# Performance work log

Measured on AMD Instinct MI355X. Metric: run time of the kernel, lower is better.

## Reference

```python
import jax, jax.numpy as jnp
import numpy as np

B, C, D, H, W = 4, 128, 16, 16, 16
HID = 128
EPS = 1e-5


def setup_inputs() -> dict:
    key = jax.random.key(0)
    ks = jax.random.split(key, 10)
    s = 1.0 / np.sqrt(C)
    return {
        "x": jax.random.normal(ks[0], (B, C, D, H, W), dtype=jnp.float32),
        "Wq": jax.random.normal(ks[1], (HID, C), dtype=jnp.float32) * s,
        "bq": jax.random.normal(ks[2], (HID,), dtype=jnp.float32) * s,
        "Wk": jax.random.normal(ks[3], (HID, C), dtype=jnp.float32) * s,
        "bk": jax.random.normal(ks[4], (HID,), dtype=jnp.float32) * s,
        "Wv": jax.random.normal(ks[5], (HID, C), dtype=jnp.float32) * s,
        "bv": jax.random.normal(ks[6], (HID,), dtype=jnp.float32) * s,
        "bn_weight": jax.random.normal(ks[7], (HID,), dtype=jnp.float32),
        "bn_bias": jax.random.normal(ks[8], (HID,), dtype=jnp.float32),
        "gamma": jax.random.normal(ks[9], (1,), dtype=jnp.float32),
    }


def reference(x, Wq, bq, Wk, bk, Wv, bv, bn_weight, bn_bias, gamma):
    b, c, d, h, w = x.shape
    n = d * h * w
    xf = x.reshape(b, c, n)  # [B, C, N]
    # 1x1 conv3d == per-voxel linear: [B, hid, N]
    q = jnp.einsum("hc,bcn->bnh", Wq, xf) + bq  # [B, N, hid] (query permuted)
    k = jnp.einsum("hc,bcn->bhn", Wk, xf) + bk[None, :, None]  # [B, hid, N]
    v = jnp.einsum("hc,bcn->bhn", Wv, xf) + bv[None, :, None]  # [B, hid, N]
    # unscaled attention scores [B, N, N], softmax over last dim
    attn = jax.nn.softmax(jnp.einsum("bih,bhj->bij", q, k), axis=-1)
    # out[b,h,i] = sum_j v[b,h,j] * attn[b,i,j]
    out = jnp.einsum("bhj,bij->bhi", v, attn)  # [B, hid, N]
    # BatchNorm3d (training mode): per-channel stats over (B, N), biased var
    mean = jnp.mean(out, axis=(0, 2), keepdims=True)
    var = jnp.mean(jnp.square(out - mean), axis=(0, 2), keepdims=True)
    out = (out - mean) * jax.lax.rsqrt(var + EPS)
    out = out * bn_weight[None, :, None] + bn_bias[None, :, None]
    out = gamma[0] * out.reshape(b, c, d, h, w) + x
    return out
```

## Files before the change

kernel.cpp:

```cpp
#include <hip/hip_runtime.h>


#define NV 4096
#define LOG2E 1.44269504088896340736f
#define EPSV 1e-5f

typedef float f32x4 __attribute__((ext_vector_type(4)));
typedef short bf16x8 __attribute__((ext_vector_type(8)));
typedef unsigned short u16x4 __attribute__((ext_vector_type(4)));
typedef unsigned short u16x8 __attribute__((ext_vector_type(8)));
typedef unsigned int u32x2 __attribute__((ext_vector_type(2)));

static __device__ __forceinline__ unsigned short f2bf(float f) {
    union { float f; unsigned u; } v; v.f = f;
    unsigned r = v.u + 0x7FFFu + ((v.u >> 16) & 1u);
    return (unsigned short)(r >> 16);
}
static __device__ __forceinline__ float bf2f(unsigned short u) {
    union { unsigned u; float f; } v; v.u = ((unsigned)u) << 16; return v.f;
}
static __device__ __forceinline__ unsigned fbits(float f) {
    union { float f; unsigned u; } v; v.f = f; return v.u;
}

__global__ __launch_bounds__(256) void projx_kernel(
    const float* __restrict__ x,
    const float* __restrict__ Wq, const float* __restrict__ Wk,
    const float* __restrict__ Wv,
    const float* __restrict__ bq, const float* __restrict__ bk,
    const float* __restrict__ bv,
    unsigned short* __restrict__ Qb, unsigned short* __restrict__ Kb,
    unsigned short* __restrict__ Vb)
{
    __shared__ unsigned short xt[64 * 136];
    __shared__ unsigned short Wl[128 * 136];
    const int bid = blockIdx.x;
    const int m = bid >> 8, b = (bid >> 6) & 3, n0 = (bid & 63) << 6;
    const int t = threadIdx.x, w = t >> 6, lane = t & 63;
    const int quad = lane >> 4, l16 = lane & 15;

    const float* Wm = (m == 0) ? Wq : ((m == 1) ? Wk : Wv);
    const float* bias = (m == 0) ? bq : ((m == 1) ? bk : bv);

    #pragma unroll
    for (int it = 0; it < 32; ++it) {
        const int e = it * 256 + t;
        const int c = e >> 6, il = e & 63;
        xt[il * 136 + c] = f2bf(x[(((b << 7) + c) << 12) + n0 + il]);
    }
    #pragma unroll
    for (int it = 0; it < 16; ++it) {
        const int idx = it * 1024 + (t << 2);
        const float4 wv4 = *(const float4*)(Wm + idx);
        const int h = idx >> 7, c = idx & 127;
        u16x4 pk;
        pk[0] = f2bf(wv4.x); pk[1] = f2bf(wv4.y);
        pk[2] = f2bf(wv4.z); pk[3] = f2bf(wv4.w);
        *(u16x4*)(Wl + h * 136 + c) = pk;
    }
    __syncthreads();

    bf16x8 af[4];
    {
        const int il = (w << 4) + l16;
        #pragma unroll
        for (int ck = 0; ck < 4; ++ck)
            af[ck] = *(const bf16x8*)(xt + il * 136 + (ck << 5) + (quad << 3));
    }
    if (m == 2) __syncthreads();

    const int vb = n0 + (w << 4);
    unsigned short* dst = (m == 0) ? Qb : Kb;
    #pragma unroll
    for (int s = 0; s < 8; ++s) {
        const int h = (s << 4) + l16;
        f32x4 acc = {0.f, 0.f, 0.f, 0.f};
        #pragma unroll
        for (int ck = 0; ck < 4; ++ck) {
            const bf16x8 wf = *(const bf16x8*)(Wl + h * 136 + (ck << 5) + (quad << 3));
            acc = __builtin_amdgcn_mfma_f32_16x16x32_bf16(af[ck], wf, acc, 0, 0, 0);
        }
        const float bval = bias[h];
        if (m == 2) {
            #pragma unroll
            for (int r = 0; r < 4; ++r)
                xt[h * 66 + (w << 4) + (quad << 2) + r] = f2bf(acc[r] + bval);
        } else {
            #pragma unroll
            for (int r = 0; r < 4; ++r) {
                float val = acc[r] + bval;
                if (m == 0) val *= LOG2E;
                const int n = vb + (quad << 2) + r;
                dst[(((b << 12) + n) << 7) + h] = f2bf(val);
            }
        }
    }
    if (m == 2) {
        __syncthreads();
        #pragma unroll
        for (int it = 0; it < 32; ++it) {
            const int e = it * 256 + t;
            const int h = e >> 6, il = e & 63;
            Vb[(((b << 7) + h) << 12) + n0 + il] = xt[h * 66 + il];
        }
    }
}

template<int NSL>
__global__ __launch_bounds__(256, 2) void flash_kernel(
    const unsigned short* __restrict__ Qb,
    const unsigned short* __restrict__ Kb,
    const unsigned short* __restrict__ Vb,
    unsigned short* __restrict__ Opart, float* __restrict__ lpart,
    unsigned short* __restrict__ Obuf)
{
    __shared__ unsigned short Kt[64 * 128];
    __shared__ unsigned short Vt[128 * 64];
    __shared__ unsigned short pA[4][32 * 72];
    const int bid = blockIdx.x;
    const int sl = bid >> 7, b = (bid >> 5) & 3, ic = bid & 31;
    const int t = threadIdx.x, w = t >> 6, lane = t & 63;
    const int quad = lane >> 4, l16 = lane & 15;
    const int iw = (ic << 7) + (w << 5);
    const int jbase = sl * (NV / NSL);
    unsigned short* pAw = pA[w];

    const int ktg = t & 15, ktj = t >> 4;
    const int vtg = t & 7,  vth = t >> 3;
    const int kswz = (ktg ^ ktj) << 3;
    const int vswz = (vtg ^ (vth & 7)) << 3;

    bf16x8 qf[2][4];
    #pragma unroll
    for (int half = 0; half < 2; ++half) {
        const unsigned short* qp =
            Qb + (((b << 12) + iw + (half << 4) + l16) << 7) + (quad << 3);
        #pragma unroll
        for (int ck = 0; ck < 4; ++ck) qf[half][ck] = *(const bf16x8*)(qp + (ck << 5));
    }
    f32x4 Oacc[2][8];
    #pragma unroll
    for (int half = 0; half < 2; ++half)
        #pragma unroll
        for (int s = 0; s < 8; ++s) Oacc[half][s] = (f32x4){0.f, 0.f, 0.f, 0.f};
    float lsum0 = 0.f, lsum1 = 0.f;

    const unsigned short* Kbb = Kb + ((long)b << 19);
    const unsigned short* Vbb = Vb + ((long)b << 19);
    const int T = (NV / NSL) >> 6;

    bf16x8 sk[4], sv[4];
    #pragma unroll
    for (int r = 0; r < 4; ++r)
        sk[r] = *(const bf16x8*)(Kbb + ((jbase + (r << 4) + ktj) << 7) + (ktg << 3));
    #pragma unroll
    for (int r = 0; r < 4; ++r)
        sv[r] = *(const bf16x8*)(Vbb + (((r << 5) + vth) << 12) + jbase + (vtg << 3));

    for (int t8 = 0; t8 < T; ++t8) {
        const int j0 = jbase + (t8 << 6);

        __syncthreads();
        #pragma unroll
        for (int r = 0; r < 4; ++r)
            *(bf16x8*)(Kt + (((r << 4) + ktj) << 7) + kswz) = sk[r];
        #pragma unroll
        for (int r = 0; r < 4; ++r)
            *(bf16x8*)(Vt + (((r << 5) + vth) << 6) + vswz) = sv[r];
        __syncthreads();

        if (t8 + 1 < T) {
            const int j1 = j0 + 64;
            #pragma unroll
            for (int r = 0; r < 4; ++r)
                sk[r] = *(const bf16x8*)(Kbb + ((j1 + (r << 4) + ktj) << 7) + (ktg << 3));
            #pragma unroll
            for (int r = 0; r < 4; ++r)
                sv[r] = *(const bf16x8*)(Vbb + (((r << 5) + vth) << 12) + j1 + (vtg << 3));
        }

        #pragma unroll
        for (int js = 0; js < 4; ++js) {
            bf16x8 kf[4];
            const int krow = ((js << 4) + l16) << 7;
            #pragma unroll
            for (int ck = 0; ck < 4; ++ck)
                kf[ck] = *(const bf16x8*)(Kt + krow + ((((ck << 2) + quad) ^ l16) << 3));
            f32x4 a0 = {0.f, 0.f, 0.f, 0.f}, a1 = {0.f, 0.f, 0.f, 0.f};
            #pragma unroll
            for (int ck = 0; ck < 4; ++ck) {
                a0 = __builtin_amdgcn_mfma_f32_16x16x32_bf16(kf[ck], qf[0][ck], a0, 0, 0, 0);
                a1 = __builtin_amdgcn_mfma_f32_16x16x32_bf16(kf[ck], qf[1][ck], a1, 0, 0, 0);
            }
            f32x4 e0, e1;
            #pragma unroll
            for (int r = 0; r < 4; ++r) {
                e0[r] = __builtin_amdgcn_exp2f(a0[r]);
                e1[r] = __builtin_amdgcn_exp2f(a1[r]);
            }
            lsum0 += (e0[0] + e0[1]) + (e0[2] + e0[3]);
            lsum1 += (e1[0] + e1[1]) + (e1[2] + e1[3]);
            u32x2 pk0, pk1;
            pk0[0] = __builtin_amdgcn_perm(fbits(e0[1]), fbits(e0[0]), 0x07060302u);
            pk0[1] = __builtin_amdgcn_perm(fbits(e0[3]), fbits(e0[2]), 0x07060302u);
            pk1[0] = __builtin_amdgcn_perm(fbits(e1[1]), fbits(e1[0]), 0x07060302u);
            pk1[1] = __builtin_amdgcn_perm(fbits(e1[3]), fbits(e1[2]), 0x07060302u);
            const int jc = (js << 4) + (quad << 2);
            *(u32x2*)(pAw + l16 * 72 + jc)        = pk0;
            *(u32x2*)(pAw + (16 + l16) * 72 + jc) = pk1;
        }
        bf16x8 pf[2][2];
        #pragma unroll
        for (int half = 0; half < 2; ++half)
            #pragma unroll
            for (int kh = 0; kh < 2; ++kh)
                pf[half][kh] = *(const bf16x8*)(pAw + ((half << 4) + l16) * 72 +
                                                (kh << 5) + (quad << 3));
        #pragma unroll
        for (int s = 0; s < 8; ++s) {
            const int vrow = ((s << 4) + l16) << 6;
            const bf16x8 v0 = *(const bf16x8*)(Vt + vrow + ((quad ^ (l16 & 7)) << 3));
            const bf16x8 v1 = *(const bf16x8*)(Vt + vrow + (((4 + quad) ^ (l16 & 7)) << 3));
            Oacc[0][s] = __builtin_amdgcn_mfma_f32_16x16x32_bf16(v0, pf[0][0], Oacc[0][s], 0, 0, 0);
            Oacc[0][s] = __builtin_amdgcn_mfma_f32_16x16x32_bf16(v1, pf[0][1], Oacc[0][s], 0, 0, 0);
            Oacc[1][s] = __builtin_amdgcn_mfma_f32_16x16x32_bf16(v0, pf[1][0], Oacc[1][s], 0, 0, 0);
            Oacc[1][s] = __builtin_amdgcn_mfma_f32_16x16x32_bf16(v1, pf[1][1], Oacc[1][s], 0, 0, 0);
        }
    }

    float l0 = lsum0; l0 += __shfl_xor(l0, 16); l0 += __shfl_xor(l0, 32);
    float l1 = lsum1; l1 += __shfl_xor(l1, 16); l1 += __shfl_xor(l1, 32);

    if (NSL == 1) {
        const float rl0 = 1.f / l0, rl1 = 1.f / l1;
        #pragma unroll
        for (int s = 0; s < 8; ++s)
            #pragma unroll
            for (int r = 0; r < 4; ++r) {
                const int h = (s << 4) + (quad << 2) + r;
                Obuf[(((b << 7) + h) << 12) + iw + l16]      = f2bf(Oacc[0][s][r] * rl0);
                Obuf[(((b << 7) + h) << 12) + iw + 16 + l16] = f2bf(Oacc[1][s][r] * rl1);
            }
    } else {
        const int slb = (sl << 2) + b;
        if (quad == 0) {
            lpart[(slb << 12) + iw + l16]      = l0;
            lpart[(slb << 12) + iw + 16 + l16] = l1;
        }
        unsigned short* Ob = Opart + ((long)slb << 19);
        #pragma unroll
        for (int half = 0; half < 2; ++half)
            #pragma unroll
            for (int s = 0; s < 8; ++s)
                #pragma unroll
                for (int r = 0; r < 4; ++r) {
                    const int h = (s << 4) + (quad << 2) + r;
                    Ob[(h << 12) + iw + (half << 4) + l16] = f2bf(Oacc[half][s][r]);
                }
    }
}

template<int NSL>
__global__ __launch_bounds__(1024) void mf_kernel(
    const unsigned short* __restrict__ Opart, const float* __restrict__ lpart,
    const float* __restrict__ x, const float* __restrict__ bnw,
    const float* __restrict__ bnb, const float* __restrict__ gammap,
    float* __restrict__ out)
{
    const int h = blockIdx.x;
    const int t = threadIdx.x;
    const int b = t >> 8;
    const int i0 = (t & 255) << 4;

    float A[16], L[16];
    #pragma unroll
    for (int k = 0; k < 16; ++k) { A[k] = 0.f; L[k] = 0.f; }
    #pragma unroll
    for (int sl = 0; sl < NSL; ++sl) {
        const int slb = (sl << 2) + b;
        const u16x8 u0 = *(const u16x8*)(Opart + ((long)slb << 19) + ((long)h << 12) + i0);
        const u16x8 u1 = *(const u16x8*)(Opart + ((long)slb << 19) + ((long)h << 12) + i0 + 8);
        const float* lp = lpart + (slb << 12) + i0;
        #pragma unroll
        for (int k = 0; k < 8; ++k) { A[k] += bf2f(u0[k]); A[8 + k] += bf2f(u1[k]); }
        #pragma unroll
        for (int k = 0; k < 4; ++k) {
            const float4 lv = *(const float4*)(lp + (k << 2));
            L[(k << 2) + 0] += lv.x; L[(k << 2) + 1] += lv.y;
            L[(k << 2) + 2] += lv.z; L[(k << 2) + 3] += lv.w;
        }
    }
    float o[16], s = 0.f, ss = 0.f;
    #pragma unroll
    for (int k = 0; k < 16; ++k) {
        o[k] = A[k] / L[k];
        s += o[k]; ss += o[k] * o[k];
    }
    #pragma unroll
    for (int off = 32; off; off >>= 1) {
        s  += __shfl_down(s, off);
        ss += __shfl_down(ss, off);
    }
    __shared__ float rs[16], rss[16], fin[2];
    const int wid = t >> 6;
    if ((t & 63) == 0) { rs[wid] = s; rss[wid] = ss; }
    __syncthreads();
    if (t == 0) {
        float s2 = 0.f, ss2 = 0.f;
        #pragma unroll
        for (int k = 0; k < 16; ++k) { s2 += rs[k]; ss2 += rss[k]; }
        fin[0] = s2; fin[1] = ss2;
    }
    __syncthreads();
    const float inv = 1.f / 16384.f;
    const float mean = fin[0] * inv;
    const float var  = fin[1] * inv - mean * mean;
    const float g = gammap[0];
    const float scale = bnw[h] * rsqrtf(var + EPSV);
    const float a  = g * scale;
    const float bb = g * (bnb[h] - mean * scale);

    const float* xp = x + (((b << 7) + h) << 12) + i0;
    float* op = out + (((b << 7) + h) << 12) + i0;
    #pragma unroll
    for (int k = 0; k < 4; ++k) {
        const float4 xv = *(const float4*)(xp + (k << 2));
        float4 r;
        r.x = o[(k << 2) + 0] * a + bb + xv.x;
        r.y = o[(k << 2) + 1] * a + bb + xv.y;
        r.z = o[(k << 2) + 2] * a + bb + xv.z;
        r.w = o[(k << 2) + 3] * a + bb + xv.w;
        *(float4*)(op + (k << 2)) = r;
    }
}

__global__ __launch_bounds__(1024) void mf1_kernel(
    const unsigned short* __restrict__ Obuf,
    const float* __restrict__ x, const float* __restrict__ bnw,
    const float* __restrict__ bnb, const float* __restrict__ gammap,
    float* __restrict__ out)
{
    const int h = blockIdx.x;
    const int t = threadIdx.x;
    const int b = t >> 8;
    const int i0 = (t & 255) << 4;
    const u16x8 u0 = *(const u16x8*)(Obuf + (((b << 7) + h) << 12) + i0);
    const u16x8 u1 = *(const u16x8*)(Obuf + (((b << 7) + h) << 12) + i0 + 8);
    float o[16], s = 0.f, ss = 0.f;
    #pragma unroll
    for (int k = 0; k < 8; ++k) { o[k] = bf2f(u0[k]); o[8 + k] = bf2f(u1[k]); }
    #pragma unroll
    for (int k = 0; k < 16; ++k) { s += o[k]; ss += o[k] * o[k]; }
    #pragma unroll
    for (int off = 32; off; off >>= 1) {
        s  += __shfl_down(s, off);
        ss += __shfl_down(ss, off);
    }
    __shared__ float rs[16], rss[16], fin[2];
    const int wid = t >> 6;
    if ((t & 63) == 0) { rs[wid] = s; rss[wid] = ss; }
    __syncthreads();
    if (t == 0) {
        float s2 = 0.f, ss2 = 0.f;
        #pragma unroll
        for (int k = 0; k < 16; ++k) { s2 += rs[k]; ss2 += rss[k]; }
        fin[0] = s2; fin[1] = ss2;
    }
    __syncthreads();
    const float inv = 1.f / 16384.f;
    const float mean = fin[0] * inv;
    const float var  = fin[1] * inv - mean * mean;
    const float g = gammap[0];
    const float scale = bnw[h] * rsqrtf(var + EPSV);
    const float a  = g * scale;
    const float bb = g * (bnb[h] - mean * scale);
    const float* xp = x + (((b << 7) + h) << 12) + i0;
    float* op = out + (((b << 7) + h) << 12) + i0;
    #pragma unroll
    for (int k = 0; k < 4; ++k) {
        const float4 xv = *(const float4*)(xp + (k << 2));
        float4 r;
        r.x = o[(k << 2) + 0] * a + bb + xv.x;
        r.y = o[(k << 2) + 1] * a + bb + xv.y;
        r.z = o[(k << 2) + 2] * a + bb + xv.z;
        r.w = o[(k << 2) + 3] * a + bb + xv.w;
        *(float4*)(op + (k << 2)) = r;
    }
}

extern "C" void kernel_launch(void* const* d_in, const int* in_sizes, int n_in,
                              void* d_out, int out_size, void* d_ws, size_t ws_size,
                              hipStream_t stream) {
    const float* x   = (const float*)d_in[0];
    const float* Wq  = (const float*)d_in[1];
    const float* bq  = (const float*)d_in[2];
    const float* Wk  = (const float*)d_in[3];
    const float* bk  = (const float*)d_in[4];
    const float* Wv  = (const float*)d_in[5];
    const float* bv  = (const float*)d_in[6];
    const float* bnw = (const float*)d_in[7];
    const float* bnb = (const float*)d_in[8];
    const float* gam = (const float*)d_in[9];
    float* out = (float*)d_out;

    char* ws = (char*)d_ws;
    unsigned short* Obuf = (unsigned short*)(ws);
    unsigned short* Qb   = (unsigned short*)(ws + (4u  << 20));
    unsigned short* Kb   = (unsigned short*)(ws + (8u  << 20));
    unsigned short* Vb   = (unsigned short*)(ws + (12u << 20));
    float*          lpart = (float*)(ws + (16u << 20) + (128u << 10));
    unsigned short* Opart = (unsigned short*)(ws + (17u << 20));

    int nsl = 1;
    if      (ws_size >= (17ull << 20) + (32ull << 20)) nsl = 8;
    else if (ws_size >= (17ull << 20) + (16ull << 20)) nsl = 4;
    else if (ws_size >= (17ull << 20) + (8ull  << 20)) nsl = 2;

    projx_kernel<<<768, 256, 0, stream>>>(x, Wq, Wk, Wv, bq, bk, bv, Qb, Kb, Vb);
    if (nsl == 8) {
        flash_kernel<8><<<1024, 256, 0, stream>>>(Qb, Kb, Vb, Opart, lpart, Obuf);
        mf_kernel<8><<<128, 1024, 0, stream>>>(Opart, lpart, x, bnw, bnb, gam, out);
    } else if (nsl == 4) {
        flash_kernel<4><<<512, 256, 0, stream>>>(Qb, Kb, Vb, Opart, lpart, Obuf);
        mf_kernel<4><<<128, 1024, 0, stream>>>(Opart, lpart, x, bnw, bnb, gam, out);
    } else if (nsl == 2) {
        flash_kernel<2><<<256, 256, 0, stream>>>(Qb, Kb, Vb, Opart, lpart, Obuf);
        mf_kernel<2><<<128, 1024, 0, stream>>>(Opart, lpart, x, bnw, bnb, gam, out);
    } else {
        flash_kernel<1><<<128, 256, 0, stream>>>(Qb, Kb, Vb, Opart, lpart, Obuf);
        mf1_kernel<<<128, 1024, 0, stream>>>(Obuf, x, bnw, bnb, gam, out);
    }
}
```

Measured before the change: 149.0 us.

## Use 6-way uneven KV split, XCD-aware block remap, MFMA priority, staged Q/K stores

The flash kernel now splits the key range into 6 uneven slices (11 or 10 tiles of 64), giving 768 blocks instead of 1024, which better matches two blocks per CU across the device. Block indices are remapped so consecutive hardware block IDs, which are distributed round-robin across the 8 XCDs, land on contiguous work and share K/V in cache. s_setprio is raised around the MFMA groups to favour the matrix-issuing wave. The projection kernel also stages Q/K results in LDS and writes them out as coalesced 16-byte rows instead of scattered 2-byte stores. Risks: the uneven slices produce load imbalance, and the combine kernel has to handle the new slice count correctly.

```diff
diff --git a/kernel.cpp b/kernel.cpp
--- a/kernel.cpp
+++ b/kernel.cpp
@@ -69,8 +69,6 @@
     }
     if (m == 2) __syncthreads();
 
-    const int vb = n0 + (w << 4);
-    unsigned short* dst = (m == 0) ? Qb : Kb;
     #pragma unroll
     for (int s = 0; s < 8; ++s) {
         const int h = (s << 4) + l16;
@@ -90,18 +88,26 @@
             for (int r = 0; r < 4; ++r) {
                 float val = acc[r] + bval;
                 if (m == 0) val *= LOG2E;
-                const int n = vb + (quad << 2) + r;
-                dst[(((b << 12) + n) << 7) + h] = f2bf(val);
+                xt[((w << 4) + (quad << 2) + r) * 136 + h] = f2bf(val);
             }
         }
     }
+    __syncthreads();
     if (m == 2) {
-        __syncthreads();
         #pragma unroll
         for (int it = 0; it < 32; ++it) {
             const int e = it * 256 + t;
             const int h = e >> 6, il = e & 63;
             Vb[(((b << 7) + h) << 12) + n0 + il] = xt[h * 66 + il];
+        }
+    } else {
+        unsigned short* dst = (m == 0) ? Qb : Kb;
+        #pragma unroll
+        for (int it = 0; it < 4; ++it) {
+            const int e = (it << 8) + t;
+            const int row = e >> 4, c8 = (e & 15) << 3;
+            *(bf16x8*)(dst + (((b << 12) + n0 + row) << 7) + c8) =
+                *(const bf16x8*)(xt + row * 136 + c8);
         }
     }
 }
@@ -117,12 +123,22 @@
     __shared__ unsigned short Kt[64 * 128];
     __shared__ unsigned short Vt[128 * 64];
     __shared__ unsigned short pA[4][32 * 72];
-    const int bid = blockIdx.x;
+    constexpr int NB = (NSL == 6) ? 768 : NSL * 128;
+    const int bid = ((blockIdx.x & 7) * (NB >> 3)) + (blockIdx.x >> 3);
     const int sl = bid >> 7, b = (bid >> 5) & 3, ic = bid & 31;
     const int t = threadIdx.x, w = t >> 6, lane = t & 63;
     const int quad = lane >> 4, l16 = lane & 15;
     const int iw = (ic << 7) + (w << 5);
-    const int jbase = sl * (NV / NSL);
+
+    int T, joff;
+    if constexpr (NSL == 6) {
+        T = 11 - (sl >= 4);
+        joff = sl * 11 - ((sl >= 5) ? 1 : 0);
+    } else {
+        T = (NV / NSL) >> 6;
+        joff = sl * T;
+    }
+    const int jbase = joff << 6;
     unsigned short* pAw = pA[w];
 
     const int ktg = t & 15, ktj = t >> 4;
@@ -147,7 +163,6 @@
 
     const unsigned short* Kbb = Kb + ((long)b << 19);
     const unsigned short* Vbb = Vb + ((long)b << 19);
-    const int T = (NV / NSL) >> 6;
 
     bf16x8 sk[4], sv[4];
     #pragma unroll
@@ -187,11 +202,13 @@
             for (int ck = 0; ck < 4; ++ck)
                 kf[ck] = *(const bf16x8*)(Kt + krow + ((((ck << 2) + quad) ^ l16) << 3));
             f32x4 a0 = {0.f, 0.f, 0.f, 0.f}, a1 = {0.f, 0.f, 0.f, 0.f};
+            __builtin_amdgcn_s_setprio(1);
             #pragma unroll
             for (int ck = 0; ck < 4; ++ck) {
                 a0 = __builtin_amdgcn_mfma_f32_16x16x32_bf16(kf[ck], qf[0][ck], a0, 0, 0, 0);
                 a1 = __builtin_amdgcn_mfma_f32_16x16x32_bf16(kf[ck], qf[1][ck], a1, 0, 0, 0);
             }
+            __builtin_amdgcn_s_setprio(0);
             f32x4 e0, e1;
             #pragma unroll
             for (int r = 0; r < 4; ++r) {
@@ -221,10 +238,12 @@
             const int vrow = ((s << 4) + l16) << 6;
             const bf16x8 v0 = *(const bf16x8*)(Vt + vrow + ((quad ^ (l16 & 7)) << 3));
             const bf16x8 v1 = *(const bf16x8*)(Vt + vrow + (((4 + quad) ^ (l16 & 7)) << 3));
+            __builtin_amdgcn_s_setprio(1);
             Oacc[0][s] = __builtin_amdgcn_mfma_f32_16x16x32_bf16(v0, pf[0][0], Oacc[0][s], 0, 0, 0);
             Oacc[0][s] = __builtin_amdgcn_mfma_f32_16x16x32_bf16(v1, pf[0][1], Oacc[0][s], 0, 0, 0);
             Oacc[1][s] = __builtin_amdgcn_mfma_f32_16x16x32_bf16(v0, pf[1][0], Oacc[1][s], 0, 0, 0);
             Oacc[1][s] = __builtin_amdgcn_mfma_f32_16x16x32_bf16(v1, pf[1][1], Oacc[1][s], 0, 0, 0);
+            __builtin_amdgcn_s_setprio(0);
         }
     }
 
@@ -412,14 +431,14 @@
     unsigned short* Opart = (unsigned short*)(ws + (17u << 20));
 
     int nsl = 1;
-    if      (ws_size >= (17ull << 20) + (32ull << 20)) nsl = 8;
+    if      (ws_size >= (17ull << 20) + (32ull << 20)) nsl = 6;
     else if (ws_size >= (17ull << 20) + (16ull << 20)) nsl = 4;
     else if (ws_size >= (17ull << 20) + (8ull  << 20)) nsl = 2;
 
     projx_kernel<<<768, 256, 0, stream>>>(x, Wq, Wk, Wv, bq, bk, bv, Qb, Kb, Vb);
-    if (nsl == 8) {
-        flash_kernel<8><<<1024, 256, 0, stream>>>(Qb, Kb, Vb, Opart, lpart, Obuf);
-        mf_kernel<8><<<128, 1024, 0, stream>>>(Opart, lpart, x, bnw, bnb, gam, out);
+    if (nsl == 6) {
+        flash_kernel<6><<<768, 256, 0, stream>>>(Qb, Kb, Vb, Opart, lpart, Obuf);
+        mf_kernel<6><<<128, 1024, 0, stream>>>(Opart, lpart, x, bnw, bnb, gam, out);
     } else if (nsl == 4) {
         flash_kernel<4><<<512, 256, 0, stream>>>(Qb, Kb, Vb, Opart, lpart, Obuf);
         mf_kernel<4><<<128, 1024, 0, stream>>>(Opart, lpart, x, bnw, bnb, gam, out);
```

After: 148.3 us. About the same (-0.4%).
